# Performance work log

Hardware: AMD Instinct MI355X
Metric: run time of the kernel (lower is better)

Reference implementation:

```python
import jax, jax.numpy as jnp
import numpy as np

W_LEN = 37  # window_length
EPS = 1e-9
LRELU_SLOPE = 0.2
SQRT2 = 1.4142135623730951


def win_sum(x, w):
    # Depthwise sliding-window sum of width w, 'same' padding w//2 (odd w).
    # Equivalent to the diag-kernel conv1d in the original code, but O(T) via cumsum.
    pad = w // 2
    xp = jnp.pad(x, ((0, 0), (0, 0), (pad, pad)))
    cs = jnp.cumsum(xp, axis=-1)
    cs = jnp.pad(cs, ((0, 0), (0, 0), (1, 0)))
    return cs[..., w:] - cs[..., :-w]


def conv1d(x, w, b):
    # x: [B,C,T], w: [O,I,3], padding=1
    y = jax.lax.conv_general_dilated(x, w, (1,), [(1, 1)],
                                     dimension_numbers=('NCH', 'OIH', 'NCH'))
    return y + b[None, :, None]


def adawin_instance(x, s, mask, fc_w, fc_b, alpha):
    # x: [B,C,T], s: [B,S,T], mask: [B,T]
    C = x.shape[1]
    h = jnp.einsum('bst,cs->bct', s, fc_w) + fc_b[None, :, None]  # [B,2C,T]
    m = mask[:, None, :]                       # [B,1,T]
    denom = win_sum(m, W_LEN) + EPS            # same for all channels
    gamma = win_sum(h[:, :C], W_LEN) / denom * m
    beta = win_sum(h[:, C:], W_LEN) / denom * m
    x_norm = jnp.tanh(alpha * x)               # WindowedNorm1d.forward
    return (1.0 + gamma) * x_norm + beta


def setup_inputs() -> dict:
    key = jax.random.key(0)
    ks = jax.random.split(key, 10)
    B, C_IN, C_OUT, S, T = 16, 512, 512, 128, 2048
    inp = {
        'x': jax.random.normal(ks[0], (B, C_IN, T), dtype=jnp.float32),
        's': jax.random.normal(ks[1], (B, S, T), dtype=jnp.float32),
        'lengths': jax.random.randint(ks[2], (B,), 0, T).astype(jnp.int32),
        'fc1_w': jax.random.normal(ks[3], (2 * C_IN, S), dtype=jnp.float32) * 0.05,
        'fc1_b': jnp.zeros((2 * C_IN,), dtype=jnp.float32),
        'alpha1': jnp.full((1,), 0.5, dtype=jnp.float32),
        'conv1_w': jax.random.normal(ks[4], (C_OUT, C_IN, 3), dtype=jnp.float32) * 0.02,
        'conv1_b': jnp.zeros((C_OUT,), dtype=jnp.float32),
        'fc2_w': jax.random.normal(ks[5], (2 * C_OUT, S), dtype=jnp.float32) * 0.05,
        'fc2_b': jnp.zeros((2 * C_OUT,), dtype=jnp.float32),
        'alpha2': jnp.full((1,), 0.5, dtype=jnp.float32),
        'conv2_w': jax.random.normal(ks[6], (C_OUT, C_OUT, 3), dtype=jnp.float32) * 0.02,
        'conv2_b': jnp.zeros((C_OUT,), dtype=jnp.float32),
    }
    return inp


def reference(x, s, lengths, fc1_w, fc1_b, alpha1, conv1_w, conv1_b,
              fc2_w, fc2_b, alpha2, conv2_w, conv2_b):
    T = x.shape[2]
    mask = (jnp.arange(T)[None, :] < lengths[:, None]).astype(x.dtype)  # [B,T]

    h = adawin_instance(x, s, mask, fc1_w, fc1_b, alpha1)
    h = jax.nn.leaky_relu(h, LRELU_SLOPE)
    h = conv1d(h, conv1_w, conv1_b)
    h = adawin_instance(h, s, mask, fc2_w, fc2_b, alpha2)
    h = jax.nn.leaky_relu(h, LRELU_SLOPE)
    h = conv1d(h, conv2_w, conv2_b)

    # dim_in == dim_out -> identity shortcut
    return (h + x) / SQRT2
```

## Files before the change

### kernel.cpp

```cpp
#include <hip/hip_runtime.h>

#define B_ 16
#define C_ 512
#define S_ 128
#define T_ 2048
#define HALF 18
#define WLEN 37

typedef __bf16 bf16x8 __attribute__((ext_vector_type(8)));
typedef float f32x4 __attribute__((ext_vector_type(4)));
typedef float f32x16 __attribute__((ext_vector_type(16)));
typedef unsigned short ushort_t;

__device__ inline ushort_t f2bf(float x) {
    unsigned u = __float_as_uint(x);
    u += 0x7fffu + ((u >> 16) & 1u);
    return (ushort_t)(u >> 16);
}
__device__ inline float bf2f(ushort_t h) {
    return __uint_as_float(((unsigned)h) << 16);
}
__device__ inline float fast_tanh(float z) {
    float e = __expf(2.f * z);
    return 1.f - __fdividef(2.f, e + 1.f);
}
__device__ __forceinline__ void glds16(const void* g, void* l) {
    __builtin_amdgcn_global_load_lds(
        (const __attribute__((address_space(1))) unsigned*)g,
        (__attribute__((address_space(3))) unsigned*)l, 16, 0, 0);
}

#define MFMA16(a, b, c) __builtin_amdgcn_mfma_f32_16x16x32_bf16((a), (b), (c), 0, 0, 0)
#define MFMA32(a, b, c) __builtin_amdgcn_mfma_f32_32x32x16_bf16((a), (b), (c), 0, 0, 0)

#define ACH_BYTES 14336
#define BCH_BYTES 7168
#define CH_BYTES (ACH_BYTES + BCH_BYTES)

__global__ __launch_bounds__(256) void prep_all(
    const float* __restrict__ s, ushort_t* __restrict__ sw_t,
    const float* __restrict__ fc1, const float* __restrict__ fc2,
    ushort_t* __restrict__ Wfc, const float* __restrict__ c1,
    const float* __restrict__ c2, ushort_t* __restrict__ I1,
    ushort_t* __restrict__ I2, ushort_t* __restrict__ y1p,
    ushort_t* __restrict__ y2p) {
    __shared__ float sb[128][101];
    int bid = blockIdx.x;
    int tid = threadIdx.x;
    if (bid < 512) {
        int b = bid >> 5;
        int t0 = (bid & 31) * 64;
        for (int e = tid; e < 128 * 100; e += 256) {
            int sj = e / 100;
            int u = e - sj * 100;
            int gt = t0 - HALF + u;
            float v = 0.f;
            if (gt >= 0 && gt < T_) v = s[((size_t)(b * S_ + sj)) * T_ + gt];
            sb[sj][u] = v;
        }
        __syncthreads();
        for (int e = tid; e < 64 * 128; e += 256) {
            int tl = e >> 7;
            int sj = e & 127;
            float sum = 0.f;
#pragma unroll
            for (int d = 0; d < WLEN; ++d) sum += sb[sj][tl + d];
            sw_t[((size_t)(b * T_ + t0 + tl)) * S_ + sj] = f2bf(sum);
        }
    } else if (bid < 1408) {
        int idx = (bid - 512) * 256 + tid;
        const int per_conv = 4 * 32 * 896;
        int conv = idx >= per_conv;
        int rr = conv ? idx - per_conv : idx;
        const float* src = conv ? c2 : c1;
        ushort_t* dst = conv ? I2 : I1;
        int chunk_id = rr / 896;
        int srem = rr - chunk_id * 896;
        int ob = chunk_id >> 5, cc = chunk_id & 31;
        int off = srem * 16;
        int row = off / 112;
        int c = off - row * 112;
        ushort_t vals[8];
        if (c >= 96) {
#pragma unroll
            for (int e = 0; e < 8; ++e) vals[e] = 0;
        } else {
            int tap = c >> 5;
            int kh8 = (c & 16) ? 8 : 0;
            int o = ob * 128 + row;
            int ibase = cc * 16 + kh8;
#pragma unroll
            for (int e = 0; e < 8; ++e)
                vals[e] = f2bf(src[(size_t)(o * 512 + ibase + e) * 3 + tap]);
        }
        uint4 pk;
        pk.x = vals[0] | ((unsigned)vals[1] << 16);
        pk.y = vals[2] | ((unsigned)vals[3] << 16);
        pk.z = vals[4] | ((unsigned)vals[5] << 16);
        pk.w = vals[6] | ((unsigned)vals[7] << 16);
        *(uint4*)&dst[(size_t)rr * 8] = pk;
    } else if (bid < 2432) {
        const int n_fc = 1024 * 128;
        int idx = (bid - 1408) * 256 + tid;
        if (idx < n_fc) Wfc[idx] = f2bf(fc1[idx]);
        else if (idx < 2 * n_fc) Wfc[idx] = f2bf(fc2[idx - n_fc]);
    } else {
        int t2 = (bid - 2432) * 256 + tid;
        if (t2 < 4096) {
            ushort_t* base = (t2 & 1) ? y2p : y1p;
            int r = t2 >> 1;
            int bb = r >> 7;
            int rowsel = (r >> 6) & 1;
            int col = (r & 63) * 8;
            size_t row = (size_t)bb * (T_ + 2) + (rowsel ? (T_ + 1) : 0);
            *(uint4*)&base[row * C_ + col] = (uint4){0, 0, 0, 0};
        }
    }
}

template <int INLAYOUT>
__global__ __launch_bounds__(256) void adawin_kernel(
    const void* __restrict__ xin_, const ushort_t* __restrict__ sw_t,
    const ushort_t* __restrict__ Wfc, const float* __restrict__ fcb,
    const float* __restrict__ alpha, const int* __restrict__ lengths,
    ushort_t* __restrict__ youtp) {
    int t0 = blockIdx.x * 64;
    int c0 = blockIdx.y * 64;
    int b = blockIdx.z;
    __shared__ __attribute__((aligned(16))) ushort_t smem[128 * 136 + 64 * 136];
    ushort_t (*As)[136] = (ushort_t(*)[136])smem;
    ushort_t (*Bs)[136] = (ushort_t(*)[136])(smem + 128 * 136);
    int tid = threadIdx.x;

    {
        int r = tid >> 4;
        int cseg = (tid & 15) * 8;
#pragma unroll
        for (int p = 0; p < 8; ++p) {
            int row = p * 16 + r;
            int grow = (row < 64) ? (c0 + row) : (448 + c0 + row);
            *(uint4*)&As[row][cseg] = *(const uint4*)&Wfc[(size_t)grow * 128 + cseg];
        }
    }
    {
        int tl = tid & 63;
        int sg = tid >> 6;
        const ushort_t* src = &sw_t[((size_t)(b * T_ + t0 + tl)) * S_];
#pragma unroll
        for (int j = 0; j < 4; ++j) {
            int col = sg * 32 + j * 8;
            *(uint4*)&Bs[tl][col] = *(const uint4*)&src[col];
        }
    }
    __syncthreads();

    int wave = tid >> 6, lane = tid & 63;
    int quad = lane >> 4, l = lane & 15;
    f32x4 accg[4], accb[4];
#pragma unroll
    for (int n = 0; n < 4; ++n) {
        accg[n] = (f32x4){0.f, 0.f, 0.f, 0.f};
        accb[n] = (f32x4){0.f, 0.f, 0.f, 0.f};
    }
    int rg = wave * 16 + l;
    int rb = 64 + wave * 16 + l;
#pragma unroll
    for (int ks = 0; ks < 4; ++ks) {
        int kc = ks * 32 + quad * 8;
        bf16x8 ag = *(const bf16x8*)&As[rg][kc];
        bf16x8 ab = *(const bf16x8*)&As[rb][kc];
#pragma unroll
        for (int n = 0; n < 4; ++n) {
            bf16x8 bb = *(const bf16x8*)&Bs[n * 16 + l][kc];
            accg[n] = MFMA16(ag, bb, accg[n]);
            accb[n] = MFMA16(ab, bb, accb[n]);
        }
    }

    __syncthreads();
    ushort_t (*Ts)[72] = (ushort_t(*)[72])smem;

    int len = lengths[b];
    float alph = alpha[0];
    const float* xf = (const float*)xin_;
    const ushort_t* xh = (const ushort_t*)xin_;
    int clocal = wave * 16 + quad * 4;
    int cbase = c0 + clocal;
#pragma unroll
    for (int n = 0; n < 4; ++n) {
        int t = t0 + n * 16 + l;
        int lo = t - HALF; if (lo < 0) lo = 0;
        int hi = t + HALF; if (hi > T_ - 1) hi = T_ - 1;
        float cnt = (float)(hi - lo + 1);
        int hv = hi < (len - 1) ? hi : (len - 1);
        int mdi = hv - lo + 1; if (mdi < 0) mdi = 0;
        float m = (t < len) ? 1.f : 0.f;
        float sc = m / ((float)mdi + 1e-9f);

        float xv[4];
        if (INLAYOUT == 0) {
#pragma unroll
            for (int j = 0; j < 4; ++j)
                xv[j] = xf[(size_t)(b * C_ + cbase + j) * T_ + t];
        } else {
            uint2 xraw = *(const uint2*)&xh[((size_t)(b * (T_ + 2) + 1 + t)) * C_ + cbase];
            xv[0] = bf2f((ushort_t)(xraw.x & 0xffff));
            xv[1] = bf2f((ushort_t)(xraw.x >> 16));
            xv[2] = bf2f((ushort_t)(xraw.y & 0xffff));
            xv[3] = bf2f((ushort_t)(xraw.y >> 16));
        }
        unsigned pk[2];
#pragma unroll
        for (int j = 0; j < 4; ++j) {
            int c = cbase + j;
            float gamma = (accg[n][j] + fcb[c] * cnt) * sc;
            float beta = (accb[n][j] + fcb[C_ + c] * cnt) * sc;
            float xn = fast_tanh(alph * xv[j]);
            float v = (1.f + gamma) * xn + beta;
            v = v > 0.f ? v : 0.2f * v;
            unsigned hv16 = (unsigned)f2bf(v);
            if (j & 1) pk[j >> 1] |= hv16 << 16;
            else pk[j >> 1] = hv16;
        }
        *(uint2*)&Ts[n * 16 + l][clocal] = (uint2){pk[0], pk[1]};
    }
    __syncthreads();
    {
        int row = tid >> 2;
        int seg = (tid & 3) * 16;
        size_t gbase = ((size_t)(b * (T_ + 2) + 1 + t0 + row)) * C_ + c0 + seg;
        *(uint4*)&youtp[gbase] = *(const uint4*)&Ts[row][seg];
        *(uint4*)&youtp[gbase + 8] = *(const uint4*)&Ts[row][seg + 8];
    }
}

__device__ __forceinline__ void stage_chunk(const char* img, const char* xt, int cc,
                                            char* Ab, char* Bb, int wave, int lane) {
#pragma unroll
    for (int k = 0; k < 6; ++k) {
        int g = wave + 4 * k;
        if (g >= 21) continue;
        if (g < 14) {
            glds16(img + g * 1024 + lane * 16, Ab + g * 1024);
        } else {
            int j = g - 14;
            int off = j * 1024 + lane * 16;
            int r = off / 48;
            int sl = (off - r * 48) >> 4;
            if (sl == 2) sl = 0;
            if (r > 129) r = 129;
            glds16(xt + (size_t)r * 1024 + cc * 32 + sl * 16, Bb + j * 1024);
        }
    }
}

template <int EPI>
__global__ __launch_bounds__(256, 3) void conv_kernel(
    const ushort_t* __restrict__ Xp, const ushort_t* __restrict__ Wimg,
    const float* __restrict__ bias, const float* __restrict__ resid,
    ushort_t* __restrict__ out_bf, float* __restrict__ out_f) {
    int t0 = blockIdx.x * 128;
    int o0 = blockIdx.y * 128;
    int b = blockIdx.z;
    __shared__ __attribute__((aligned(16))) char smem[2 * CH_BYTES];
    int tid = threadIdx.x;
    int lane = tid & 63, wave = tid >> 6;
    int l32 = lane & 31, khalf = lane >> 5;
    int wo = (wave & 1) * 64, wt = (wave >> 1) * 64;

    const char* imgbase = (const char*)Wimg + (size_t)blockIdx.y * 32 * ACH_BYTES;
    const char* xt = (const char*)Xp + (size_t)(b * (T_ + 2) + t0) * 1024;

    f32x16 acc[2][2];
#pragma unroll
    for (int io = 0; io < 2; ++io)
#pragma unroll
        for (int it = 0; it < 2; ++it)
#pragma unroll
            for (int r = 0; r < 16; ++r) acc[io][it][r] = 0.f;

    stage_chunk(imgbase, xt, 0, smem, smem + ACH_BYTES, wave, lane);

#pragma unroll 1
    for (int c = 0; c < 32; ++c) {
        int cur = c & 1;
        char* Ab = smem + cur * CH_BYTES;
        if (c < 31) {
            char* An = smem + (cur ^ 1) * CH_BYTES;
            stage_chunk(imgbase + (size_t)(c + 1) * ACH_BYTES, xt, c + 1,
                        An, An + ACH_BYTES, wave, lane);
            if (wave == 0) asm volatile("s_waitcnt vmcnt(6)\ns_barrier" ::: "memory");
            else           asm volatile("s_waitcnt vmcnt(5)\ns_barrier" ::: "memory");
        } else {
            asm volatile("s_waitcnt vmcnt(0)\ns_barrier" ::: "memory");
        }
        ushort_t (*As)[56] = (ushort_t(*)[56])Ab;
        ushort_t (*Bs)[24] = (ushort_t(*)[24])(Ab + ACH_BYTES);
#pragma unroll
        for (int p = 0; p < 3; ++p) {
            bf16x8 a0 = *(const bf16x8*)&As[wo + l32][p * 16 + khalf * 8];
            bf16x8 a1 = *(const bf16x8*)&As[wo + 32 + l32][p * 16 + khalf * 8];
            bf16x8 b0 = *(const bf16x8*)&Bs[wt + l32 + p][khalf * 8];
            bf16x8 b1 = *(const bf16x8*)&Bs[wt + 32 + l32 + p][khalf * 8];
            acc[0][0] = MFMA32(a0, b0, acc[0][0]);
            acc[0][1] = MFMA32(a0, b1, acc[0][1]);
            acc[1][0] = MFMA32(a1, b0, acc[1][0]);
            acc[1][1] = MFMA32(a1, b1, acc[1][1]);
        }
        asm volatile("s_barrier" ::: "memory");
    }

    if (EPI == 0) {
        ushort_t (*Ts)[136] = (ushort_t(*)[136])smem;
#pragma unroll
        for (int io = 0; io < 2; ++io)
#pragma unroll
            for (int it = 0; it < 2; ++it) {
                int trow = wt + it * 32 + l32;
#pragma unroll
                for (int g = 0; g < 4; ++g) {
                    int oc = wo + io * 32 + g * 8 + khalf * 4;
                    unsigned pk[2];
#pragma unroll
                    for (int j = 0; j < 4; ++j) {
                        float v = acc[io][it][g * 4 + j] + bias[o0 + oc + j];
                        unsigned hv16 = (unsigned)f2bf(v);
                        if (j & 1) pk[j >> 1] |= hv16 << 16;
                        else pk[j >> 1] = hv16;
                    }
                    *(uint2*)&Ts[trow][oc] = (uint2){pk[0], pk[1]};
                }
            }
        __syncthreads();
        int cc = (tid & 15) * 8;
        int rbse = tid >> 4;
#pragma unroll
        for (int j = 0; j < 8; ++j) {
            int row = j * 16 + rbse;
            *(uint4*)&out_bf[((size_t)(b * (T_ + 2) + 1 + t0 + row)) * C_ + o0 + cc] =
                *(const uint4*)&Ts[row][cc];
        }
    } else {
#pragma unroll
        for (int io = 0; io < 2; ++io)
#pragma unroll
            for (int it = 0; it < 2; ++it) {
                int obase = o0 + wo + io * 32;
                int t = t0 + wt + it * 32 + l32;
#pragma unroll
                for (int g = 0; g < 4; ++g) {
                    int oo = obase + g * 8 + khalf * 4;
#pragma unroll
                    for (int j = 0; j < 4; ++j) {
                        size_t off = (size_t)(b * C_ + oo + j) * T_ + t;
                        out_f[off] = (acc[io][it][g * 4 + j] + bias[oo + j] + resid[off]) *
                                     0.70710678118654752f;
                    }
                }
            }
    }
}

extern "C" void kernel_launch(void* const* d_in, const int* in_sizes, int n_in,
                              void* d_out, int out_size, void* d_ws, size_t ws_size,
                              hipStream_t stream) {
    const float* x = (const float*)d_in[0];
    const float* s = (const float*)d_in[1];
    const int* lengths = (const int*)d_in[2];
    const float* fc1_w = (const float*)d_in[3];
    const float* fc1_b = (const float*)d_in[4];
    const float* alpha1 = (const float*)d_in[5];
    const float* conv1_w = (const float*)d_in[6];
    const float* conv1_b = (const float*)d_in[7];
    const float* fc2_w = (const float*)d_in[8];
    const float* fc2_b = (const float*)d_in[9];
    const float* alpha2 = (const float*)d_in[10];
    const float* conv2_w = (const float*)d_in[11];
    const float* conv2_b = (const float*)d_in[12];

    const size_t IMGB = (size_t)4 * 32 * ACH_BYTES;
    char* ws = (char*)d_ws;
    ushort_t* sw_t = (ushort_t*)ws; ws += (size_t)B_ * T_ * S_ * 2;
    ushort_t* Wfc = (ushort_t*)ws;  ws += (size_t)2 * 1024 * 128 * 2;
    ushort_t* I1 = (ushort_t*)ws;   ws += IMGB;
    ushort_t* I2 = (ushort_t*)ws;   ws += IMGB;
    ushort_t* y2p = (ushort_t*)ws;  ws += (size_t)B_ * (T_ + 2) * C_ * 2;
    ushort_t* y1p = (ushort_t*)ws;  ws += (size_t)B_ * (T_ + 2) * C_ * 2;
    ws += 12 * 1024;
    if ((size_t)(ws - (char*)d_ws) > ws_size) return;

    prep_all<<<dim3(2448), dim3(256), 0, stream>>>(
        s, sw_t, fc1_w, fc2_w, Wfc, conv1_w, conv2_w, I1, I2, y1p, y2p);
    adawin_kernel<0><<<dim3(32, 8, 16), dim3(256), 0, stream>>>(
        (const void*)x, sw_t, Wfc, fc1_b, alpha1, lengths, y1p);
    conv_kernel<0><<<dim3(16, 4, 16), dim3(256), 0, stream>>>(
        y1p, I1, conv1_b, (const float*)nullptr, y2p, (float*)nullptr);
    adawin_kernel<1><<<dim3(32, 8, 16), dim3(256), 0, stream>>>(
        (const void*)y2p, sw_t, Wfc + 1024 * 128, fc2_b, alpha2, lengths, y1p);
    conv_kernel<1><<<dim3(16, 4, 16), dim3(256), 0, stream>>>(
        y1p, I2, conv2_b, x, (ushort_t*)nullptr, (float*)d_out);
}
```

Baseline: 354.5 us.

## Load conv weight fragments directly into registers instead of staging through LDS

The conv kernel now reads weight (A) fragments for each input-channel chunk straight from global memory into registers, prefetched two chunks ahead. Only the activation (B) tile is double-buffered in LDS. The weight image drops its padding columns (112 to 96 per row), which shrinks the prep work and the image size. This cuts LDS traffic and LDS footprint per block, which may allow more occupancy. In exchange it raises VGPR pressure and issues uncoalesced 16-byte global loads per lane, with a more intricate vmcnt/barrier schedule.

```diff
diff --git a/kernel.cpp b/kernel.cpp
--- a/kernel.cpp
+++ b/kernel.cpp
@@ -33,9 +33,8 @@
 #define MFMA16(a, b, c) __builtin_amdgcn_mfma_f32_16x16x32_bf16((a), (b), (c), 0, 0, 0)
 #define MFMA32(a, b, c) __builtin_amdgcn_mfma_f32_32x32x16_bf16((a), (b), (c), 0, 0, 0)
 
-#define ACH_BYTES 14336
+#define AIMG_CH 12288
 #define BCH_BYTES 7168
-#define CH_BYTES (ACH_BYTES + BCH_BYTES)
 
 __global__ __launch_bounds__(256) void prep_all(
     const float* __restrict__ s, ushort_t* __restrict__ sw_t,
@@ -67,45 +66,40 @@
             for (int d = 0; d < WLEN; ++d) sum += sb[sj][tl + d];
             sw_t[((size_t)(b * T_ + t0 + tl)) * S_ + sj] = f2bf(sum);
         }
-    } else if (bid < 1408) {
+    } else if (bid < 1280) {
         int idx = (bid - 512) * 256 + tid;
-        const int per_conv = 4 * 32 * 896;
+        const int per_conv = 4 * 32 * 768;
         int conv = idx >= per_conv;
         int rr = conv ? idx - per_conv : idx;
         const float* src = conv ? c2 : c1;
         ushort_t* dst = conv ? I2 : I1;
-        int chunk_id = rr / 896;
-        int srem = rr - chunk_id * 896;
+        int chunk_id = rr / 768;
+        int srem = rr - chunk_id * 768;
         int ob = chunk_id >> 5, cc = chunk_id & 31;
-        int off = srem * 16;
-        int row = off / 112;
-        int c = off - row * 112;
+        int row = srem / 6;
+        int sl = srem - row * 6;
+        int c = sl * 16;
+        int tap = c >> 5;
+        int kh8 = (c & 16) ? 8 : 0;
+        int o = ob * 128 + row;
+        int ibase = cc * 16 + kh8;
         ushort_t vals[8];
-        if (c >= 96) {
-#pragma unroll
-            for (int e = 0; e < 8; ++e) vals[e] = 0;
-        } else {
-            int tap = c >> 5;
-            int kh8 = (c & 16) ? 8 : 0;
-            int o = ob * 128 + row;
-            int ibase = cc * 16 + kh8;
-#pragma unroll
-            for (int e = 0; e < 8; ++e)
-                vals[e] = f2bf(src[(size_t)(o * 512 + ibase + e) * 3 + tap]);
-        }
+#pragma unroll
+        for (int e = 0; e < 8; ++e)
+            vals[e] = f2bf(src[(size_t)(o * 512 + ibase + e) * 3 + tap]);
         uint4 pk;
         pk.x = vals[0] | ((unsigned)vals[1] << 16);
         pk.y = vals[2] | ((unsigned)vals[3] << 16);
         pk.z = vals[4] | ((unsigned)vals[5] << 16);
         pk.w = vals[6] | ((unsigned)vals[7] << 16);
         *(uint4*)&dst[(size_t)rr * 8] = pk;
-    } else if (bid < 2432) {
+    } else if (bid < 2304) {
         const int n_fc = 1024 * 128;
-        int idx = (bid - 1408) * 256 + tid;
+        int idx = (bid - 1280) * 256 + tid;
         if (idx < n_fc) Wfc[idx] = f2bf(fc1[idx]);
         else if (idx < 2 * n_fc) Wfc[idx] = f2bf(fc2[idx - n_fc]);
     } else {
-        int t2 = (bid - 2432) * 256 + tid;
+        int t2 = (bid - 2304) * 256 + tid;
         if (t2 < 4096) {
             ushort_t* base = (t2 & 1) ? y2p : y1p;
             int r = t2 >> 1;
@@ -234,25 +228,34 @@
     }
 }
 
-__device__ __forceinline__ void stage_chunk(const char* img, const char* xt, int cc,
-                                            char* Ab, char* Bb, int wave, int lane) {
-#pragma unroll
-    for (int k = 0; k < 6; ++k) {
+__device__ __forceinline__ void stage_b(const char* xt, int cc, char* Bb,
+                                        int wave, int lane) {
+#pragma unroll
+    for (int k = 0; k < 2; ++k) {
         int g = wave + 4 * k;
-        if (g >= 21) continue;
-        if (g < 14) {
-            glds16(img + g * 1024 + lane * 16, Ab + g * 1024);
-        } else {
-            int j = g - 14;
-            int off = j * 1024 + lane * 16;
-            int r = off / 48;
-            int sl = (off - r * 48) >> 4;
-            if (sl == 2) sl = 0;
-            if (r > 129) r = 129;
-            glds16(xt + (size_t)r * 1024 + cc * 32 + sl * 16, Bb + j * 1024);
-        }
-    }
-}
+        if (g >= 7) continue;
+        int off = g * 1024 + lane * 16;
+        int r = off / 48;
+        int sl = (off - r * 48) >> 4;
+        if (sl == 2) sl = 0;
+        if (r > 129) r = 129;
+        glds16(xt + (size_t)r * 1024 + cc * 32 + sl * 16, Bb + g * 1024);
+    }
+}
+
+#define LOAD_A(dst, img)                                                        \
+    {                                                                           \
+        _Pragma("unroll") for (int io = 0; io < 2; ++io)                        \
+            _Pragma("unroll") for (int p = 0; p < 3; ++p)                       \
+                dst[io * 3 + p] =                                               \
+                    *(const bf16x8*)((img) + aoff[io * 3 + p]);                 \
+    }
+
+#define WAITC()                                                                  \
+    {                                                                            \
+        if (wave == 3) asm volatile("s_waitcnt vmcnt(7)" ::: "memory");          \
+        else asm volatile("s_waitcnt vmcnt(8)" ::: "memory");                    \
+    }
 
 template <int EPI>
 __global__ __launch_bounds__(256, 3) void conv_kernel(
@@ -262,14 +265,23 @@
     int t0 = blockIdx.x * 128;
     int o0 = blockIdx.y * 128;
     int b = blockIdx.z;
-    __shared__ __attribute__((aligned(16))) char smem[2 * CH_BYTES];
+    __shared__ __attribute__((aligned(16))) char smem[34816];
     int tid = threadIdx.x;
     int lane = tid & 63, wave = tid >> 6;
     int l32 = lane & 31, khalf = lane >> 5;
     int wo = (wave & 1) * 64, wt = (wave >> 1) * 64;
 
-    const char* imgbase = (const char*)Wimg + (size_t)blockIdx.y * 32 * ACH_BYTES;
+    const char* imgbase = (const char*)Wimg + (size_t)blockIdx.y * 32 * AIMG_CH;
     const char* xt = (const char*)Xp + (size_t)(b * (T_ + 2) + t0) * 1024;
+    char* buf0 = smem;
+    char* buf1 = smem + BCH_BYTES;
+
+    int aoff[6];
+#pragma unroll
+    for (int io = 0; io < 2; ++io)
+#pragma unroll
+        for (int p = 0; p < 3; ++p)
+            aoff[io * 3 + p] = (wo + io * 32 + l32) * 96 + p * 32 + khalf * 16;
 
     f32x16 acc[2][2];
 #pragma unroll
@@ -279,33 +291,58 @@
 #pragma unroll
             for (int r = 0; r < 16; ++r) acc[io][it][r] = 0.f;
 
-    stage_chunk(imgbase, xt, 0, smem, smem + ACH_BYTES, wave, lane);
+    bf16x8 a0r[6], a1r[6];
+
+    LOAD_A(a0r, imgbase);
+    stage_b(xt, 0, buf0, wave, lane);
+    LOAD_A(a1r, imgbase + AIMG_CH);
+    stage_b(xt, 1, buf1, wave, lane);
+    WAITC();
+    asm volatile("s_barrier" ::: "memory");
 
 #pragma unroll 1
-    for (int c = 0; c < 32; ++c) {
-        int cur = c & 1;
-        char* Ab = smem + cur * CH_BYTES;
-        if (c < 31) {
-            char* An = smem + (cur ^ 1) * CH_BYTES;
-            stage_chunk(imgbase + (size_t)(c + 1) * ACH_BYTES, xt, c + 1,
-                        An, An + ACH_BYTES, wave, lane);
-            if (wave == 0) asm volatile("s_waitcnt vmcnt(6)\ns_barrier" ::: "memory");
-            else           asm volatile("s_waitcnt vmcnt(5)\ns_barrier" ::: "memory");
+    for (int i = 0; i < 16; ++i) {
+        int e = 2 * i;
+        {
+            ushort_t (*Bs)[24] = (ushort_t(*)[24])buf0;
+#pragma unroll
+            for (int p = 0; p < 3; ++p) {
+                bf16x8 b0 = *(const bf16x8*)&Bs[wt + l32 + p][khalf * 8];
+                bf16x8 b1 = *(const bf16x8*)&Bs[wt + 32 + l32 + p][khalf * 8];
+                acc[0][0] = MFMA32(a0r[p], b0, acc[0][0]);
+                acc[0][1] = MFMA32(a0r[p], b1, acc[0][1]);
+                acc[1][0] = MFMA32(a0r[3 + p], b0, acc[1][0]);
+                acc[1][1] = MFMA32(a0r[3 + p], b1, acc[1][1]);
+            }
+        }
+        asm volatile("s_barrier" ::: "memory");
+        if (e + 2 < 32) {
+            LOAD_A(a0r, imgbase + (size_t)(e + 2) * AIMG_CH);
+            stage_b(xt, e + 2, buf0, wave, lane);
+            WAITC();
         } else {
-            asm volatile("s_waitcnt vmcnt(0)\ns_barrier" ::: "memory");
-        }
-        ushort_t (*As)[56] = (ushort_t(*)[56])Ab;
-        ushort_t (*Bs)[24] = (ushort_t(*)[24])(Ab + ACH_BYTES);
-#pragma unroll
-        for (int p = 0; p < 3; ++p) {
-            bf16x8 a0 = *(const bf16x8*)&As[wo + l32][p * 16 + khalf * 8];
-            bf16x8 a1 = *(const bf16x8*)&As[wo + 32 + l32][p * 16 + khalf * 8];
-            bf16x8 b0 = *(const bf16x8*)&Bs[wt + l32 + p][khalf * 8];
-            bf16x8 b1 = *(const bf16x8*)&Bs[wt + 32 + l32 + p][khalf * 8];
-            acc[0][0] = MFMA32(a0, b0, acc[0][0]);
-            acc[0][1] = MFMA32(a0, b1, acc[0][1]);
-            acc[1][0] = MFMA32(a1, b0, acc[1][0]);
-            acc[1][1] = MFMA32(a1, b1, acc[1][1]);
+            asm volatile("s_waitcnt vmcnt(0)" ::: "memory");
+        }
+        asm volatile("s_barrier" ::: "memory");
+        {
+            ushort_t (*Bs)[24] = (ushort_t(*)[24])buf1;
+#pragma unroll
+            for (int p = 0; p < 3; ++p) {
+                bf16x8 b0 = *(const bf16x8*)&Bs[wt + l32 + p][khalf * 8];
+                bf16x8 b1 = *(const bf16x8*)&Bs[wt + 32 + l32 + p][khalf * 8];
+                acc[0][0] = MFMA32(a1r[p], b0, acc[0][0]);
+                acc[0][1] = MFMA32(a1r[p], b1, acc[0][1]);
+                acc[1][0] = MFMA32(a1r[3 + p], b0, acc[1][0]);
+                acc[1][1] = MFMA32(a1r[3 + p], b1, acc[1][1]);
+            }
+        }
+        asm volatile("s_barrier" ::: "memory");
+        if (e + 3 < 32) {
+            LOAD_A(a1r, imgbase + (size_t)(e + 3) * AIMG_CH);
+            stage_b(xt, e + 3, buf1, wave, lane);
+            WAITC();
+        } else {
+            asm volatile("s_waitcnt vmcnt(0)" ::: "memory");
         }
         asm volatile("s_barrier" ::: "memory");
     }
@@ -378,7 +415,7 @@
     const float* conv2_w = (const float*)d_in[11];
     const float* conv2_b = (const float*)d_in[12];
 
-    const size_t IMGB = (size_t)4 * 32 * ACH_BYTES;
+    const size_t IMGB = (size_t)4 * 32 * AIMG_CH;
     char* ws = (char*)d_ws;
     ushort_t* sw_t = (ushort_t*)ws; ws += (size_t)B_ * T_ * S_ * 2;
     ushort_t* Wfc = (ushort_t*)ws;  ws += (size_t)2 * 1024 * 128 * 2;
@@ -389,7 +426,7 @@
     ws += 12 * 1024;
     if ((size_t)(ws - (char*)d_ws) > ws_size) return;
 
-    prep_all<<<dim3(2448), dim3(256), 0, stream>>>(
+    prep_all<<<dim3(2320), dim3(256), 0, stream>>>(
         s, sw_t, fc1_w, fc2_w, Wfc, conv1_w, conv2_w, I1, I2, y1p, y2p);
     adawin_kernel<0><<<dim3(32, 8, 16), dim3(256), 0, stream>>>(
         (const void*)x, sw_t, Wfc, fc1_b, alpha1, lengths, y1p);
```

New measurement: 395.5 us. +11.6%, slower.
